# Kernel optimization log

Hardware: AMD Instinct MI355X
Metric: run time of the kernel (lower is better)

Reference implementation:

```python
import jax, jax.numpy as jnp
from jax import lax
import numpy as np

H = 16   # num_heads
K = 31   # kernel_size
P = 15   # padding_l (left padding for 'same')


def setup_inputs() -> dict:
    key = jax.random.key(0)
    k1, k2, k3 = jax.random.split(key, 3)
    T, B, C = 2048, 32, 512
    x = jax.random.normal(k1, (T, B, C), dtype=jnp.float32)
    # xavier-uniform-ish init for (H, 1, K)
    limit = float(np.sqrt(6.0 / (1 + K)))
    weight = jax.random.uniform(k2, (H, 1, K), dtype=jnp.float32, minval=-limit, maxval=limit)
    bias = jnp.zeros((C,), dtype=jnp.float32)
    return {"x": x, "weight": weight, "bias": bias}


def reference(x, weight, bias):
    # x: (T, B, C); weight: (H, 1, K); bias: (C,)
    T, B, C = x.shape
    R = C // H  # channels per head
    w = weight.reshape(H, K)
    # weight_softmax=True: softmax over kernel dim in fp32, cast back
    w = jax.nn.softmax(w.astype(jnp.float32), axis=1).astype(weight.dtype)
    # expand per-head weights to per-channel depthwise kernel (C, 1, K)
    wc = jnp.repeat(w, R, axis=0)[:, None, :]
    x_bct = jnp.transpose(x, (1, 2, 0))  # (B, C, T)
    # out[b,c,t] = sum_k wc[c,0,k] * x[b,c,t - P + k], zero-padded
    out = lax.conv_general_dilated(
        x_bct, wc,
        window_strides=(1,),
        padding=[(P, K - 1 - P)],
        feature_group_count=C,
        dimension_numbers=("NCH", "OIH", "NCH"),
    )  # (B, C, T)
    out = jnp.transpose(out, (2, 0, 1))  # (T, B, C)
    return out + bias[None, None, :]
```

## Files before the change

### kernel.cpp

```cpp
#include <hip/hip_runtime.h>

#define T_DIM 2048
#define B_DIM 32
#define C_DIM 512
#define H_DIM 16
#define K_DIM 31
#define P_PAD 15
#define TT 32
#define JN (TT + K_DIM - 1)
#define NCOL (B_DIM * C_DIM)

__global__ __launch_bounds__(256, 4)
void lwconv_kernel(const float* __restrict__ x, const float* __restrict__ weight,
                   const float* __restrict__ bias, float* __restrict__ out)
{
    const int wid  = __builtin_amdgcn_readfirstlane((int)(threadIdx.x >> 6));
    const int lane = threadIdx.x & 63;
    const int gw   = blockIdx.x * 4 + wid;
    const int h    = gw & (H_DIM - 1);
    const int bp   = (gw >> 4) & 15;
    const int tblk = gw >> 8;
    const int c    = (h << 5) | (lane & 31);
    const int b    = (bp << 1) | (lane >> 5);
    const int col  = b * C_DIM + c;

    float w[K_DIM];
    float m = -3.4e38f;
    #pragma unroll
    for (int k = 0; k < K_DIM; ++k) { w[k] = weight[h * K_DIM + k]; m = fmaxf(m, w[k]); }
    float s = 0.f;
    #pragma unroll
    for (int k = 0; k < K_DIM; ++k) { w[k] = __expf(w[k] - m); s += w[k]; }
    const float inv = 1.f / s;
    unsigned int ws[K_DIM];
    #pragma unroll
    for (int k = 0; k < K_DIM; ++k)
        ws[k] = __builtin_amdgcn_readfirstlane(__float_as_uint(w[k] * inv));

    const float bv = bias[c];
    const int tb = tblk * TT;
    const float* xp = x + col;
    float*       op = out + col;

    float acc[TT];
    #pragma unroll
    for (int i = 0; i < TT; ++i) acc[i] = bv;

    #pragma unroll
    for (int j = 0; j < JN; ++j) {
        const int t  = tb - P_PAD + j;
        int tc = t < 0 ? 0 : (t >= T_DIM ? T_DIM - 1 : t);
        float v = xp[(size_t)tc * NCOL];
        if (t < 0 || t >= T_DIM) v = 0.f;
        const int ilo = (j - (K_DIM - 1)) > 0 ? (j - (K_DIM - 1)) : 0;
        const int ihi = j < (TT - 1) ? j : (TT - 1);
        #pragma unroll
        for (int i = ilo; i <= ihi; ++i)
            acc[i] = fmaf(__uint_as_float(ws[j - i]), v, acc[i]);
    }

    #pragma unroll
    for (int i = 0; i < TT; ++i)
        __builtin_nontemporal_store(acc[i], &op[(size_t)(tb + i) * NCOL]);
}

extern "C" void kernel_launch(void* const* d_in, const int* in_sizes, int n_in,
                              void* d_out, int out_size, void* d_ws, size_t ws_size,
                              hipStream_t stream) {
    const float* x      = (const float*)d_in[0];
    const float* weight = (const float*)d_in[1];
    const float* bias   = (const float*)d_in[2];
    float* out = (float*)d_out;
    dim3 grid(H_DIM * 16 * (T_DIM / TT) / 4);
    dim3 block(256);
    lwconv_kernel<<<grid, block, 0, stream>>>(x, weight, bias, out);
}
```

Measured before the change: 52.52 us.

## Software-pipeline interior tile loads with inline-asm double buffering

Interior time tiles now take a separate path that issues global loads through inline assembly in batches of 16. Two register buffers alternate, and explicit s_waitcnt vmcnt calls let FMAs on one batch overlap the loads still in flight for the next. Addresses use a 32-bit offset with a scalar base, and the clamping and zeroing logic is dropped for these tiles. The two edge tiles keep the original bounds-checked loop. The path issues two extra loads per tile that no FMA uses, and the manual waitcnt ordering depends on the compiler not adding memory operations of its own in between.

```diff
diff --git a/kernel.cpp b/kernel.cpp
--- a/kernel.cpp
+++ b/kernel.cpp
@@ -7,8 +7,8 @@
 #define K_DIM 31
 #define P_PAD 15
 #define TT 32
-#define JN (TT + K_DIM - 1)
 #define NCOL (B_DIM * C_DIM)
+#define TSTEP 65536u
 
 __global__ __launch_bounds__(256, 4)
 void lwconv_kernel(const float* __restrict__ x, const float* __restrict__ weight,
@@ -39,25 +39,73 @@
 
     const float bv = bias[c];
     const int tb = tblk * TT;
-    const float* xp = x + col;
-    float*       op = out + col;
+    float* op = out + col;
 
     float acc[TT];
     #pragma unroll
     for (int i = 0; i < TT; ++i) acc[i] = bv;
 
-    #pragma unroll
-    for (int j = 0; j < JN; ++j) {
-        const int t  = tb - P_PAD + j;
-        int tc = t < 0 ? 0 : (t >= T_DIM ? T_DIM - 1 : t);
-        float v = xp[(size_t)tc * NCOL];
-        if (t < 0 || t >= T_DIM) v = 0.f;
-        const int ilo = (j - (K_DIM - 1)) > 0 ? (j - (K_DIM - 1)) : 0;
-        const int ihi = j < (TT - 1) ? j : (TT - 1);
+#define FMAS(J, V)                                                        \
+    {                                                                     \
+        const int ilo = ((J) - (K_DIM - 1)) > 0 ? ((J) - (K_DIM - 1)) : 0;\
+        const int ihi = (J) < (TT - 1) ? (J) : (TT - 1);                  \
+        _Pragma("unroll")                                                 \
+        for (int i = ilo; i <= ihi; ++i)                                  \
+            acc[i] = fmaf(__uint_as_float(ws[(J) - i]), (V), acc[i]);     \
+    }
+
+    if (tblk == 0 || tblk == (T_DIM / TT) - 1) {
+        const float* xp = x + col;
         #pragma unroll
-        for (int i = ilo; i <= ihi; ++i)
-            acc[i] = fmaf(__uint_as_float(ws[j - i]), v, acc[i]);
+        for (int j = 0; j < TT + K_DIM - 1; ++j) {
+            const int t  = tb - P_PAD + j;
+            int tc = t < 0 ? 0 : (t >= T_DIM ? T_DIM - 1 : t);
+            float v = xp[(size_t)tc * NCOL];
+            if (t < 0 || t >= T_DIM) v = 0.f;
+            FMAS(j, v);
+        }
+    } else {
+        const unsigned long long xb = (unsigned long long)(const void*)x;
+        unsigned int voff = ((unsigned)col << 2) + (unsigned)(tb - P_PAD) * TSTEP;
+        float A[16], Bv[16];
+
+#define ISSUE16(BUF)                                                      \
+        _Pragma("unroll")                                                 \
+        for (int u = 0; u < 16; ++u) {                                    \
+            asm volatile("global_load_dword %0, %1, %2"                   \
+                         : "=v"(BUF[u]) : "v"(voff), "s"(xb));            \
+            voff += TSTEP;                                                \
+        }
+
+#define WAITB(N, BUF)                                                     \
+        asm volatile("s_waitcnt vmcnt(" #N ")"                            \
+                : "+v"(BUF[0]), "+v"(BUF[1]), "+v"(BUF[2]),  "+v"(BUF[3]),\
+                  "+v"(BUF[4]), "+v"(BUF[5]), "+v"(BUF[6]),  "+v"(BUF[7]),\
+                  "+v"(BUF[8]), "+v"(BUF[9]), "+v"(BUF[10]), "+v"(BUF[11]),\
+                  "+v"(BUF[12]),"+v"(BUF[13]),"+v"(BUF[14]), "+v"(BUF[15]));
+
+#define FMA16(BASE, BUF)                                                  \
+        _Pragma("unroll")                                                 \
+        for (int u = 0; u < 16; ++u) { FMAS((BASE) + u, BUF[u]); }
+
+        ISSUE16(A);
+        ISSUE16(Bv);
+        WAITB(16, A);
+        FMA16(0, A);
+        ISSUE16(A);
+        WAITB(16, Bv);
+        FMA16(16, Bv);
+        ISSUE16(Bv);
+        WAITB(16, A);
+        FMA16(32, A);
+        WAITB(0, Bv);
+        FMA16(48, Bv);
+
+#undef ISSUE16
+#undef WAITB
+#undef FMA16
     }
+#undef FMAS
 
     #pragma unroll
     for (int i = 0; i < TT; ++i)
```

After: 50.59 us (median of 2 runs). 3.7% less time.
